# Performance work log

Hardware: AMD Instinct MI355X
Metric: run time of the kernel (lower is better)

The kernel has to match this reference:

```python
import jax, jax.numpy as jnp
import numpy as np

BS, C, H, W = 2, 128, 80, 160
P, G = 9, 8
GC = C // G
EPS = 1e-5


def _layernorm_c(x, g, b):
    # x: (bs, C, H, W); LayerNorm over channel dim (to_3d dim=2 -> norm over c)
    m = jnp.mean(x, axis=1, keepdims=True)
    v = jnp.mean((x - m) ** 2, axis=1, keepdims=True)
    return (x - m) / jnp.sqrt(v + EPS) * g[None, :, None, None] + b[None, :, None, None]


def _conv1x1(x, w, b):
    return jnp.einsum('bchw,oc->bohw', x, w) + b[None, :, None, None]


def _bilinear_sample(feat, pts):
    # feat (bs,C,H,W); pts (bs,N,2) normalized [0,1]; zero padding outside (DAF convention)
    bs, c, h, w = feat.shape
    x = pts[..., 0] * w - 0.5
    y = pts[..., 1] * h - 0.5
    x0 = jnp.floor(x)
    y0 = jnp.floor(y)
    dx = x - x0
    dy = y - y0
    x0i = x0.astype(jnp.int32)
    y0i = y0.astype(jnp.int32)

    def corner(xi, yi, wgt):
        valid = (xi >= 0) & (xi < w) & (yi >= 0) & (yi < h)
        xc = jnp.clip(xi, 0, w - 1)
        yc = jnp.clip(yi, 0, h - 1)
        g = jax.vmap(lambda f, yy, xx: f[:, yy, xx].T)(feat, yc, xc)  # (bs,N,C)
        return g * (wgt * valid)[..., None]

    return (corner(x0i, y0i, (1 - dx) * (1 - dy))
            + corner(x0i + 1, y0i, dx * (1 - dy))
            + corner(x0i, y0i + 1, (1 - dx) * dy)
            + corner(x0i + 1, y0i + 1, dx * dy))


def _branch(match_flat, anchor, feat_value, wmap, kp_w, kp_b):
    bs = feat_value.shape[0]
    hw = H * W
    # Sparse1DKeyPointsGenerator: learned 1D offsets along the disparity (x) direction
    off = match_flat @ kp_w.T + kp_b  # (bs, HW, P)
    anc = anchor.reshape(bs, hw, P, 2)
    kp = jnp.stack([anc[..., 0] + off, anc[..., 1]], axis=-1)  # (bs,HW,P,2)
    # group-softmax attention weights over num_pts
    wts = wmap.transpose(0, 2, 3, 1).reshape(bs, hw, P, G)  # channel c = p*G + g
    wts = jax.nn.softmax(wts, axis=2)
    # deformable aggregation: bilinear gather at key points + group-weighted sum over pts
    sampled = _bilinear_sample(feat_value, kp.reshape(bs, hw * P, 2))
    sampled = sampled.reshape(bs, hw, P, G, GC)
    out = jnp.einsum('bnpgc,bnpg->bngc', sampled, wts).reshape(bs, hw, C)
    out = out.reshape(bs, H, W, C).transpose(0, 3, 1, 2)
    return out, kp


def _forward(mask, match, context, geometric, context_anchor_points, geometric_anchor_points,
             ln_g, ln_b, lnc_g, lnc_b, lng_g, lng_b,
             wc_w, wc_b, wg_w, wg_b, vc_w, vc_b, vg_w, vg_b,
             out_w, out_b, kpc_w, kpc_b, kpg_w, kpg_b):
    bs = match.shape[0]
    hw = H * W
    match_n = _layernorm_c(match, ln_g, ln_b)
    context_n = _layernorm_c(context, lnc_g, lnc_b)
    geometric_n = _layernorm_c(geometric, lng_g, lng_b)
    ctx_val = _conv1x1(context_n, vc_w, vc_b)
    geo_val = _conv1x1(geometric_n, vg_w, vg_b)
    match_flat = match_n.reshape(bs, C, hw).transpose(0, 2, 1)  # (bs,HW,C)
    wc = _conv1x1(match_n, wc_w, wc_b)  # (bs,G*P,H,W)
    wg = _conv1x1(match_n, wg_w, wg_b)
    ctx_out, ctx_kp = _branch(match_flat, context_anchor_points, ctx_val, wc, kpc_w, kpc_b)
    geo_out, geo_kp = _branch(match_flat, geometric_anchor_points, geo_val, wg, kpg_w, kpg_b)
    out = jnp.concatenate([ctx_out * mask, geo_out], axis=1)
    out = _conv1x1(out, out_w, out_b)  # proj_drop is identity (p=0)
    return out, ctx_kp.reshape(bs, H, W, P, 2), geo_kp.reshape(bs, H, W, P, 2)


def setup_inputs() -> dict:
    key = jax.random.key(0)
    ks = jax.random.split(key, 20)

    def wn(k, shape):
        return jax.random.normal(k, shape, jnp.float32) * 0.02

    return {
        'mask': jax.random.uniform(ks[0], (BS, 1, H, W), jnp.float32),
        'match': jax.random.normal(ks[1], (BS, C, H, W), jnp.float32),
        'context': jax.random.normal(ks[2], (BS, C, H, W), jnp.float32),
        'geometric': jax.random.normal(ks[3], (BS, C, H, W), jnp.float32),
        'context_anchor_points': jax.random.uniform(ks[4], (BS, H, W, P, 2), jnp.float32),
        'geometric_anchor_points': jax.random.uniform(ks[5], (BS, H, W, P, 2), jnp.float32),
        'ln_g': jnp.ones((C,), jnp.float32), 'ln_b': jnp.zeros((C,), jnp.float32),
        'lnc_g': jnp.ones((C,), jnp.float32), 'lnc_b': jnp.zeros((C,), jnp.float32),
        'lng_g': jnp.ones((C,), jnp.float32), 'lng_b': jnp.zeros((C,), jnp.float32),
        'wc_w': wn(ks[6], (G * P, C)), 'wc_b': jnp.zeros((G * P,), jnp.float32),
        'wg_w': wn(ks[7], (G * P, C)), 'wg_b': jnp.zeros((G * P,), jnp.float32),
        'vc_w': wn(ks[8], (C, C)), 'vc_b': jnp.zeros((C,), jnp.float32),
        'vg_w': wn(ks[9], (C, C)), 'vg_b': jnp.zeros((C,), jnp.float32),
        'out_w': wn(ks[10], (C, 2 * C)), 'out_b': jnp.zeros((C,), jnp.float32),
        'kpc_w': wn(ks[11], (P, C)), 'kpc_b': jnp.zeros((P,), jnp.float32),
        'kpg_w': wn(ks[12], (P, C)), 'kpg_b': jnp.zeros((P,), jnp.float32),
    }


def reference(mask, match, context, geometric, context_anchor_points, geometric_anchor_points,
              ln_g, ln_b, lnc_g, lnc_b, lng_g, lng_b,
              wc_w, wc_b, wg_w, wg_b, vc_w, vc_b, vg_w, vg_b,
              out_w, out_b, kpc_w, kpc_b, kpg_w, kpg_b):
    return _forward(mask, match, context, geometric, context_anchor_points, geometric_anchor_points,
                    ln_g, ln_b, lnc_g, lnc_b, lng_g, lng_b,
                    wc_w, wc_b, wg_w, wg_b, vc_w, vc_b, vg_w, vg_b,
                    out_w, out_b, kpc_w, kpc_b, kpg_w, kpg_b)
```

## Files before the change

### kernel.cpp

```cpp
#include <hip/hip_runtime.h>
#include <hip/hip_bf16.h>

typedef __hip_bfloat16 bf16;
typedef __bf16 b16x8 __attribute__((ext_vector_type(8)));
typedef float f32x4 __attribute__((ext_vector_type(4)));

#define HWs   12800
#define NPIX  25600
#define IMG_H 80
#define IMG_W 160

static __device__ inline b16x8 load_w8(const float* p)
{
    const float4* q = (const float4*)p;
    float4 a = q[0], b = q[1];
    b16x8 r;
    r[0] = (__bf16)a.x; r[1] = (__bf16)a.y; r[2] = (__bf16)a.z; r[3] = (__bf16)a.w;
    r[4] = (__bf16)b.x; r[5] = (__bf16)b.y; r[6] = (__bf16)b.z; r[7] = (__bf16)b.w;
    return r;
}

__global__ __launch_bounds__(256) void k_stage1(
    const float* __restrict__ match, const float* __restrict__ context, const float* __restrict__ geometric,
    const float* __restrict__ ln_g, const float* __restrict__ ln_b,
    const float* __restrict__ lnc_g, const float* __restrict__ lnc_b,
    const float* __restrict__ lng_g, const float* __restrict__ lng_b,
    const float* __restrict__ vc_w, const float* __restrict__ vc_b,
    const float* __restrict__ vg_w, const float* __restrict__ vg_b,
    const float* __restrict__ wc_w, const float* __restrict__ wc_b,
    const float* __restrict__ wg_w, const float* __restrict__ wg_b,
    const float* __restrict__ kpc_w, const float* __restrict__ kpc_b,
    const float* __restrict__ kpg_w, const float* __restrict__ kpg_b,
    const float* __restrict__ anc_c, const float* __restrict__ anc_g,
    bf16* __restrict__ ctx_val, bf16* __restrict__ geo_val,
    bf16* __restrict__ wts_g, float* __restrict__ coords_g,
    float* __restrict__ kp_out)
{
    __shared__ __align__(16) bf16 tile_s[32 * 136];
    __shared__ bf16 logit_s[32 * 144];
    __shared__ float offs_s[32 * 18];
    __shared__ float red1[8][32];
    __shared__ float red2[8][32];

    int bx = blockIdx.x;
    int seg = bx / 800;
    int tile = bx - seg * 800;
    int t = threadIdx.x;
    int pixbase = tile * 32;

    const float* X  = (seg == 0) ? context : (seg == 1) ? geometric : match;
    const float* gg = (seg == 0) ? lnc_g   : (seg == 1) ? lng_g     : ln_g;
    const float* bb = (seg == 0) ? lnc_b   : (seg == 1) ? lng_b     : ln_b;

    {
        int p = t & 31;
        int cq = t >> 5;
        int b = pixbase >= HWs;
        int hw = pixbase - b * HWs;
        const float* base = X + ((size_t)b * 128) * HWs + hw + p;
        float xv[16];
        float s1 = 0.f, s2 = 0.f;
#pragma unroll
        for (int j = 0; j < 16; j++) {
            int c = cq * 16 + j;
            float v = base[(size_t)c * HWs];
            xv[j] = v; s1 += v; s2 += v * v;
        }
        red1[cq][p] = s1; red2[cq][p] = s2;
        __syncthreads();
        float S1 = 0.f, S2 = 0.f;
#pragma unroll
        for (int q = 0; q < 8; q++) { S1 += red1[q][p]; S2 += red2[q][p]; }
        float mean = S1 * (1.f / 128.f);
        float var  = fmaxf(S2 * (1.f / 128.f) - mean * mean, 0.f);
        float rstd = rsqrtf(var + 1e-5f);
#pragma unroll
        for (int j = 0; j < 16; j++) {
            int c = cq * 16 + j;
            float y = (xv[j] - mean) * rstd * gg[c] + bb[c];
            tile_s[p * 136 + c] = __float2bfloat16(y);
        }
        __syncthreads();
    }

    int wv = t >> 6;
    int lane = t & 63;
    int s = wv >> 1;
    int h = wv & 1;
    int lrow = lane & 15;
    int lq = lane >> 4;
    const b16x8* arow = (const b16x8*)(tile_s + (s * 16 + lrow) * 136);
    b16x8 af[4];
#pragma unroll
    for (int kk = 0; kk < 4; kk++) af[kk] = arow[kk * 4 + lq];

    if (seg < 2) {
        const float* Wv = (seg == 0) ? vc_w : vg_w;
        const float* Bv = (seg == 0) ? vc_b : vg_b;
        bf16* val = (seg == 0) ? ctx_val : geo_val;
#pragma unroll
        for (int i = 0; i < 4; i++) {
            int o = (h + 2 * i) * 16 + lrow;
            const float* wrow = Wv + (size_t)o * 128;
            f32x4 acc = {0.f, 0.f, 0.f, 0.f};
#pragma unroll
            for (int kk = 0; kk < 4; kk++)
                acc = __builtin_amdgcn_mfma_f32_16x16x32_bf16(af[kk], load_w8(wrow + (kk * 4 + lq) * 8), acc, 0, 0, 0);
            float bias = Bv[o];
#pragma unroll
            for (int r = 0; r < 4; r++) {
                int pix = pixbase + s * 16 + lq * 4 + r;
                val[(size_t)pix * 128 + o] = __float2bfloat16(acc[r] + bias);
            }
        }
        return;
    }

    for (int ot = h; ot < 11; ot += 2) {
        int o = ot * 16 + lrow;
        const float* wr; float bias;
        if (o < 72)       { wr = wc_w  + (size_t)o * 128;         bias = wc_b[o]; }
        else if (o < 144) { wr = wg_w  + (size_t)(o - 72) * 128;  bias = wg_b[o - 72]; }
        else if (o < 153) { wr = kpc_w + (size_t)(o - 144) * 128; bias = kpc_b[o - 144]; }
        else if (o < 162) { wr = kpg_w + (size_t)(o - 153) * 128; bias = kpg_b[o - 153]; }
        else              { wr = kpg_w + (size_t)8 * 128;         bias = 0.f; }
        f32x4 acc = {0.f, 0.f, 0.f, 0.f};
#pragma unroll
        for (int kk = 0; kk < 4; kk++)
            acc = __builtin_amdgcn_mfma_f32_16x16x32_bf16(af[kk], load_w8(wr + (kk * 4 + lq) * 8), acc, 0, 0, 0);
#pragma unroll
        for (int r = 0; r < 4; r++) {
            int row = s * 16 + lq * 4 + r;
            float v = acc[r] + bias;
            if (o < 144)       logit_s[row * 144 + o] = __float2bfloat16(v);
            else if (o < 162)  offs_s[row * 18 + (o - 144)] = v;
        }
    }
    __syncthreads();

#pragma unroll
    for (int i = 0; i < 2; i++) {
        int task = t + 256 * i;
        int lp = task >> 4;
        int sub = task & 15;
        int br = sub >> 3;
        int g = sub & 7;
        const bf16* base = logit_s + lp * 144 + br * 72 + g;
        float v[9];
        float m = -1e30f;
#pragma unroll
        for (int p = 0; p < 9; p++) { v[p] = __bfloat162float(base[p * 8]); m = fmaxf(m, v[p]); }
        float ssum = 0.f;
#pragma unroll
        for (int p = 0; p < 9; p++) { v[p] = __expf(v[p] - m); ssum += v[p]; }
        float inv = 1.f / ssum;
        int pix = pixbase + lp;
        bf16* wb = wts_g + ((size_t)pix * 2 + br) * 72 + g * 9;
#pragma unroll
        for (int p = 0; p < 9; p++) wb[p] = __float2bfloat16(v[p] * inv);
    }

    for (int i = 0; i < 3; i++) {
        int task = t + 256 * i;
        if (task < 576) {
            int lp = task / 18;
            int sub = task - lp * 18;
            int br = sub / 9;
            int p = sub - br * 9;
            int pix = pixbase + lp;
            float off = offs_s[lp * 18 + br * 9 + p];
            const float* anc = br ? anc_g : anc_c;
            float ax = anc[(size_t)pix * 18 + p * 2];
            float ay = anc[(size_t)pix * 18 + p * 2 + 1];
            float kx = ax + off;
            float* kpo = kp_out + (size_t)br * (NPIX * 18) + (size_t)pix * 18 + p * 2;
            kpo[0] = kx;
            kpo[1] = ay;
            float* cbp = coords_g + ((size_t)pix * 2 + br) * 18 + p * 2;
            cbp[0] = kx * 160.f - 0.5f;
            cbp[1] = ay * 80.f - 0.5f;
        }
    }
}

__global__ __launch_bounds__(256) void k_agg(
    const bf16* __restrict__ ctx_val, const bf16* __restrict__ geo_val,
    const bf16* __restrict__ wts_g, const float* __restrict__ coords_g,
    const float* __restrict__ mask,
    bf16* __restrict__ aggf)
{
    int t = threadIdx.x;
    int wv = t >> 6;
    int lane = t & 63;
    int q = lane >> 4;
    int sub = lane & 15;
    int c0 = sub * 8;
    int g = sub >> 1;

    int bx = blockIdx.x;
    int xcd = bx & 7;
    int br = xcd >> 2;
    int grp = (bx >> 3) * 4 + (xcd & 3);
    int pix = grp * 16 + wv * 4 + q;
    int tk = pix * 2 + br;
    int b = pix >= HWs;
    int rowbase = b * HWs;

    const bf16* val = br ? geo_val : ctx_val;
    const float* cb = coords_g + (size_t)tk * 18;
    const bf16* wb = wts_g + (size_t)tk * 72 + g * 9;

    float wtv[9];
#pragma unroll
    for (int p = 0; p < 9; p++) wtv[p] = __bfloat162float(wb[p]);

    float acc[8] = {0.f, 0.f, 0.f, 0.f, 0.f, 0.f, 0.f, 0.f};
    for (int p = 0; p < 9; p++) {
        float px = cb[p * 2];
        float py = cb[p * 2 + 1];
        float fx = floorf(px), fy = floorf(py);
        float dx = px - fx, dy = py - fy;
        int x0 = (int)fx, y0 = (int)fy;
        float wt = wtv[p];
#pragma unroll
        for (int c4 = 0; c4 < 4; c4++) {
            int xi = x0 + (c4 & 1);
            int yi = y0 + (c4 >> 1);
            bool ok = (xi >= 0) & (xi < IMG_W) & (yi >= 0) & (yi < IMG_H);
            int xc = min(max(xi, 0), IMG_W - 1);
            int yc = min(max(yi, 0), IMG_H - 1);
            float wx = (c4 & 1) ? dx : 1.f - dx;
            float wy = (c4 >> 1) ? dy : 1.f - dy;
            float wgt = ok ? wx * wy * wt : 0.f;
            b16x8 v = *(const b16x8*)(val + (size_t)(rowbase + yc * IMG_W + xc) * 128 + c0);
#pragma unroll
            for (int j = 0; j < 8; j++) acc[j] += wgt * (float)v[j];
        }
    }
    float mv = (br == 0) ? mask[pix] : 1.f;
    b16x8 pk;
#pragma unroll
    for (int j = 0; j < 8; j++) pk[j] = (__bf16)(acc[j] * mv);
    *(b16x8*)(aggf + (size_t)pix * 256 + br * 128 + c0) = pk;
}

__global__ __launch_bounds__(256) void k_gemm_out(
    const bf16* __restrict__ aggf,
    const float* __restrict__ out_w, const float* __restrict__ out_b,
    float* __restrict__ out)
{
    int t = threadIdx.x;
    int pixbase = blockIdx.x * 32;
    int wv = t >> 6;
    int lane = t & 63;
    int s = wv >> 1;
    int h = wv & 1;
    int lrow = lane & 15;
    int lq = lane >> 4;
    const b16x8* arow = (const b16x8*)(aggf + (size_t)(pixbase + s * 16 + lrow) * 256);
    b16x8 af[8];
#pragma unroll
    for (int kk = 0; kk < 8; kk++) af[kk] = arow[kk * 4 + lq];
    int b = pixbase >= HWs;
#pragma unroll
    for (int i = 0; i < 4; i++) {
        int o = (h + 2 * i) * 16 + lrow;
        const float* wrow = out_w + (size_t)o * 256;
        f32x4 acc = {0.f, 0.f, 0.f, 0.f};
#pragma unroll
        for (int kk = 0; kk < 8; kk++)
            acc = __builtin_amdgcn_mfma_f32_16x16x32_bf16(af[kk], load_w8(wrow + (kk * 4 + lq) * 8), acc, 0, 0, 0);
        float bias = out_b[o];
#pragma unroll
        for (int r = 0; r < 4; r++) {
            int pix = pixbase + s * 16 + lq * 4 + r;
            int hw = pix - b * HWs;
            out[(size_t)b * (128 * HWs) + (size_t)o * HWs + hw] = acc[r] + bias;
        }
    }
}

extern "C" void kernel_launch(void* const* d_in, const int* in_sizes, int n_in,
                              void* d_out, int out_size, void* d_ws, size_t ws_size,
                              hipStream_t stream)
{
    const float* mask      = (const float*)d_in[0];
    const float* match     = (const float*)d_in[1];
    const float* context   = (const float*)d_in[2];
    const float* geometric = (const float*)d_in[3];
    const float* anc_c     = (const float*)d_in[4];
    const float* anc_g     = (const float*)d_in[5];
    const float* ln_g  = (const float*)d_in[6];
    const float* ln_b  = (const float*)d_in[7];
    const float* lnc_g = (const float*)d_in[8];
    const float* lnc_b = (const float*)d_in[9];
    const float* lng_g = (const float*)d_in[10];
    const float* lng_b = (const float*)d_in[11];
    const float* wc_w  = (const float*)d_in[12];
    const float* wc_b  = (const float*)d_in[13];
    const float* wg_w  = (const float*)d_in[14];
    const float* wg_b  = (const float*)d_in[15];
    const float* vc_w  = (const float*)d_in[16];
    const float* vc_b  = (const float*)d_in[17];
    const float* vg_w  = (const float*)d_in[18];
    const float* vg_b  = (const float*)d_in[19];
    const float* out_w = (const float*)d_in[20];
    const float* out_b = (const float*)d_in[21];
    const float* kpc_w = (const float*)d_in[22];
    const float* kpc_b = (const float*)d_in[23];
    const float* kpg_w = (const float*)d_in[24];
    const float* kpg_b = (const float*)d_in[25];

    char* w = (char*)d_ws;
    bf16*  ctx_val  = (bf16*)(w);
    bf16*  geo_val  = (bf16*)(w + 6553600);
    bf16*  wts_g    = (bf16*)(w + 13107200);
    float* coords_g = (float*)(w + 20480000);
    bf16*  aggf     = (bf16*)(w + 24166400);

    float* outp = (float*)d_out;
    float* kp_out = outp + (size_t)2 * 128 * HWs;

    k_stage1<<<2400, 256, 0, stream>>>(match, context, geometric,
                                       ln_g, ln_b, lnc_g, lnc_b, lng_g, lng_b,
                                       vc_w, vc_b, vg_w, vg_b,
                                       wc_w, wc_b, wg_w, wg_b,
                                       kpc_w, kpc_b, kpg_w, kpg_b,
                                       anc_c, anc_g,
                                       ctx_val, geo_val, wts_g, coords_g, kp_out);
    k_agg<<<3200, 256, 0, stream>>>(ctx_val, geo_val, wts_g, coords_g, mask, aggf);
    k_gemm_out<<<800, 256, 0, stream>>>(aggf, out_w, out_b, outp);
}
```

Baseline: 238.6 us.

## Pre-convert weights to bf16, prefetch them early, fuse aggregation with output GEMM

Adds a prep kernel that converts all projection weights to bf16 and packs the matched-branch weights and biases into one contiguous buffer. Stage 1 now loads its weight fragments before the LayerNorm reduction so the loads overlap with the input loads. The aggregation and output GEMM are fused into one kernel that keeps the aggregated features in shared memory, so the aggf buffer no longer goes to and from global memory. The fused kernel runs 800 blocks with four sampling tasks per thread, down from 3200 blocks, which reduces parallelism for the latency-bound gather and drops the old XCD-aware block mapping.

```diff
diff --git a/kernel.cpp b/kernel.cpp
--- a/kernel.cpp
+++ b/kernel.cpp
@@ -10,14 +10,45 @@
 #define IMG_H 80
 #define IMG_W 160
 
-static __device__ inline b16x8 load_w8(const float* p)
+#define OFF_VCB  0
+#define OFF_VGB  16384
+#define OFF_MATB 32768
+#define OFF_OUTB 53504
+#define NW_BF16  86272
+
+__global__ __launch_bounds__(256) void k_prep(
+    const float* __restrict__ vc_w, const float* __restrict__ vg_w,
+    const float* __restrict__ wc_w, const float* __restrict__ wg_w,
+    const float* __restrict__ kpc_w, const float* __restrict__ kpg_w,
+    const float* __restrict__ out_w,
+    const float* __restrict__ wc_b, const float* __restrict__ wg_b,
+    const float* __restrict__ kpc_b, const float* __restrict__ kpg_b,
+    bf16* __restrict__ wbuf, float* __restrict__ bias176)
 {
-    const float4* q = (const float4*)p;
-    float4 a = q[0], b = q[1];
-    b16x8 r;
-    r[0] = (__bf16)a.x; r[1] = (__bf16)a.y; r[2] = (__bf16)a.z; r[3] = (__bf16)a.w;
-    r[4] = (__bf16)b.x; r[5] = (__bf16)b.y; r[6] = (__bf16)b.z; r[7] = (__bf16)b.w;
-    return r;
+    int i = blockIdx.x * 256 + threadIdx.x;
+    if (i < 16384) {
+        wbuf[i] = __float2bfloat16(vc_w[i]);
+    } else if (i < 32768) {
+        wbuf[i] = __float2bfloat16(vg_w[i - 16384]);
+    } else if (i < 53504) {
+        int j = i - 32768; int row = j >> 7; int c = j & 127;
+        float v;
+        if (row < 72)       v = wc_w[row * 128 + c];
+        else if (row < 144) v = wg_w[(row - 72) * 128 + c];
+        else if (row < 153) v = kpc_w[(row - 144) * 128 + c];
+        else                v = kpg_w[(row - 153) * 128 + c];
+        wbuf[i] = __float2bfloat16(v);
+    } else if (i < NW_BF16) {
+        wbuf[i] = __float2bfloat16(out_w[i - 53504]);
+    } else if (i < NW_BF16 + 176) {
+        int j = i - NW_BF16;
+        float v = 0.f;
+        if (j < 72)       v = wc_b[j];
+        else if (j < 144) v = wg_b[j - 72];
+        else if (j < 153) v = kpc_b[j - 144];
+        else if (j < 162) v = kpg_b[j - 153];
+        bias176[j] = v;
+    }
 }
 
 __global__ __launch_bounds__(256) void k_stage1(
@@ -25,12 +56,8 @@
     const float* __restrict__ ln_g, const float* __restrict__ ln_b,
     const float* __restrict__ lnc_g, const float* __restrict__ lnc_b,
     const float* __restrict__ lng_g, const float* __restrict__ lng_b,
-    const float* __restrict__ vc_w, const float* __restrict__ vc_b,
-    const float* __restrict__ vg_w, const float* __restrict__ vg_b,
-    const float* __restrict__ wc_w, const float* __restrict__ wc_b,
-    const float* __restrict__ wg_w, const float* __restrict__ wg_b,
-    const float* __restrict__ kpc_w, const float* __restrict__ kpc_b,
-    const float* __restrict__ kpg_w, const float* __restrict__ kpg_b,
+    const float* __restrict__ vc_b, const float* __restrict__ vg_b,
+    const bf16* __restrict__ wbuf, const float* __restrict__ bias176,
     const float* __restrict__ anc_c, const float* __restrict__ anc_g,
     bf16* __restrict__ ctx_val, bf16* __restrict__ geo_val,
     bf16* __restrict__ wts_g, float* __restrict__ coords_g,
@@ -52,36 +79,14 @@
     const float* gg = (seg == 0) ? lnc_g   : (seg == 1) ? lng_g     : ln_g;
     const float* bb = (seg == 0) ? lnc_b   : (seg == 1) ? lng_b     : ln_b;
 
-    {
-        int p = t & 31;
-        int cq = t >> 5;
-        int b = pixbase >= HWs;
-        int hw = pixbase - b * HWs;
-        const float* base = X + ((size_t)b * 128) * HWs + hw + p;
-        float xv[16];
-        float s1 = 0.f, s2 = 0.f;
-#pragma unroll
-        for (int j = 0; j < 16; j++) {
-            int c = cq * 16 + j;
-            float v = base[(size_t)c * HWs];
-            xv[j] = v; s1 += v; s2 += v * v;
-        }
-        red1[cq][p] = s1; red2[cq][p] = s2;
-        __syncthreads();
-        float S1 = 0.f, S2 = 0.f;
-#pragma unroll
-        for (int q = 0; q < 8; q++) { S1 += red1[q][p]; S2 += red2[q][p]; }
-        float mean = S1 * (1.f / 128.f);
-        float var  = fmaxf(S2 * (1.f / 128.f) - mean * mean, 0.f);
-        float rstd = rsqrtf(var + 1e-5f);
-#pragma unroll
-        for (int j = 0; j < 16; j++) {
-            int c = cq * 16 + j;
-            float y = (xv[j] - mean) * rstd * gg[c] + bb[c];
-            tile_s[p * 136 + c] = __float2bfloat16(y);
-        }
-        __syncthreads();
-    }
+    int p = t & 31;
+    int cq = t >> 5;
+    int b = pixbase >= HWs;
+    int hw = pixbase - b * HWs;
+    const float* base = X + ((size_t)b * 128) * HWs + hw + p;
+    float xv[16];
+#pragma unroll
+    for (int j = 0; j < 16; j++) xv[j] = base[(size_t)(cq * 16 + j) * HWs];
 
     int wv = t >> 6;
     int lane = t & 63;
@@ -89,45 +94,86 @@
     int h = wv & 1;
     int lrow = lane & 15;
     int lq = lane >> 4;
+    const bf16* Wb = (seg == 0) ? wbuf + OFF_VCB
+                   : (seg == 1) ? wbuf + OFF_VGB
+                                : wbuf + OFF_MATB;
+    b16x8 wf[4][4];
+    float bpre[4];
+#pragma unroll
+    for (int i = 0; i < 4; i++) {
+        int o = (h + 2 * i) * 16 + lrow;
+        const bf16* wr = Wb + (size_t)o * 128;
+#pragma unroll
+        for (int kk = 0; kk < 4; kk++)
+            wf[i][kk] = *(const b16x8*)(wr + (kk * 4 + lq) * 8);
+        bpre[i] = (seg == 0) ? vc_b[o] : (seg == 1) ? vg_b[o] : bias176[o];
+    }
+
+    {
+        float s1 = 0.f, s2 = 0.f;
+#pragma unroll
+        for (int j = 0; j < 16; j++) { s1 += xv[j]; s2 += xv[j] * xv[j]; }
+        red1[cq][p] = s1; red2[cq][p] = s2;
+        __syncthreads();
+        float S1 = 0.f, S2 = 0.f;
+#pragma unroll
+        for (int q = 0; q < 8; q++) { S1 += red1[q][p]; S2 += red2[q][p]; }
+        float mean = S1 * (1.f / 128.f);
+        float var  = fmaxf(S2 * (1.f / 128.f) - mean * mean, 0.f);
+        float rstd = rsqrtf(var + 1e-5f);
+#pragma unroll
+        for (int j = 0; j < 16; j++) {
+            int c = cq * 16 + j;
+            float y = (xv[j] - mean) * rstd * gg[c] + bb[c];
+            tile_s[p * 136 + c] = __float2bfloat16(y);
+        }
+        __syncthreads();
+    }
+
     const b16x8* arow = (const b16x8*)(tile_s + (s * 16 + lrow) * 136);
     b16x8 af[4];
 #pragma unroll
     for (int kk = 0; kk < 4; kk++) af[kk] = arow[kk * 4 + lq];
 
     if (seg < 2) {
-        const float* Wv = (seg == 0) ? vc_w : vg_w;
-        const float* Bv = (seg == 0) ? vc_b : vg_b;
         bf16* val = (seg == 0) ? ctx_val : geo_val;
 #pragma unroll
         for (int i = 0; i < 4; i++) {
             int o = (h + 2 * i) * 16 + lrow;
-            const float* wrow = Wv + (size_t)o * 128;
             f32x4 acc = {0.f, 0.f, 0.f, 0.f};
 #pragma unroll
             for (int kk = 0; kk < 4; kk++)
-                acc = __builtin_amdgcn_mfma_f32_16x16x32_bf16(af[kk], load_w8(wrow + (kk * 4 + lq) * 8), acc, 0, 0, 0);
-            float bias = Bv[o];
+                acc = __builtin_amdgcn_mfma_f32_16x16x32_bf16(af[kk], wf[i][kk], acc, 0, 0, 0);
 #pragma unroll
             for (int r = 0; r < 4; r++) {
                 int pix = pixbase + s * 16 + lq * 4 + r;
-                val[(size_t)pix * 128 + o] = __float2bfloat16(acc[r] + bias);
+                val[(size_t)pix * 128 + o] = __float2bfloat16(acc[r] + bpre[i]);
             }
         }
         return;
     }
 
-    for (int ot = h; ot < 11; ot += 2) {
+#pragma unroll
+    for (int i = 0; i < 4; i++) {
+        int o = (h + 2 * i) * 16 + lrow;
+        f32x4 acc = {0.f, 0.f, 0.f, 0.f};
+#pragma unroll
+        for (int kk = 0; kk < 4; kk++)
+            acc = __builtin_amdgcn_mfma_f32_16x16x32_bf16(af[kk], wf[i][kk], acc, 0, 0, 0);
+#pragma unroll
+        for (int r = 0; r < 4; r++) {
+            int row = s * 16 + lq * 4 + r;
+            logit_s[row * 144 + o] = __float2bfloat16(acc[r] + bpre[i]);
+        }
+    }
+    for (int ot = h + 8; ot < 11; ot += 2) {
         int o = ot * 16 + lrow;
-        const float* wr; float bias;
-        if (o < 72)       { wr = wc_w  + (size_t)o * 128;         bias = wc_b[o]; }
-        else if (o < 144) { wr = wg_w  + (size_t)(o - 72) * 128;  bias = wg_b[o - 72]; }
-        else if (o < 153) { wr = kpc_w + (size_t)(o - 144) * 128; bias = kpc_b[o - 144]; }
-        else if (o < 162) { wr = kpg_w + (size_t)(o - 153) * 128; bias = kpg_b[o - 153]; }
-        else              { wr = kpg_w + (size_t)8 * 128;         bias = 0.f; }
+        const bf16* wr = Wb + (size_t)o * 128;
         f32x4 acc = {0.f, 0.f, 0.f, 0.f};
 #pragma unroll
         for (int kk = 0; kk < 4; kk++)
-            acc = __builtin_amdgcn_mfma_f32_16x16x32_bf16(af[kk], load_w8(wr + (kk * 4 + lq) * 8), acc, 0, 0, 0);
+            acc = __builtin_amdgcn_mfma_f32_16x16x32_bf16(af[kk], *(const b16x8*)(wr + (kk * 4 + lq) * 8), acc, 0, 0, 0);
+        float bias = bias176[o];
 #pragma unroll
         for (int r = 0; r < 4; r++) {
             int row = s * 16 + lq * 4 + r;
@@ -145,19 +191,19 @@
         int sub = task & 15;
         int br = sub >> 3;
         int g = sub & 7;
-        const bf16* base = logit_s + lp * 144 + br * 72 + g;
+        const bf16* basel = logit_s + lp * 144 + br * 72 + g;
         float v[9];
         float m = -1e30f;
 #pragma unroll
-        for (int p = 0; p < 9; p++) { v[p] = __bfloat162float(base[p * 8]); m = fmaxf(m, v[p]); }
+        for (int pp = 0; pp < 9; pp++) { v[pp] = __bfloat162float(basel[pp * 8]); m = fmaxf(m, v[pp]); }
         float ssum = 0.f;
 #pragma unroll
-        for (int p = 0; p < 9; p++) { v[p] = __expf(v[p] - m); ssum += v[p]; }
+        for (int pp = 0; pp < 9; pp++) { v[pp] = __expf(v[pp] - m); ssum += v[pp]; }
         float inv = 1.f / ssum;
         int pix = pixbase + lp;
-        bf16* wb = wts_g + ((size_t)pix * 2 + br) * 72 + g * 9;
-#pragma unroll
-        for (int p = 0; p < 9; p++) wb[p] = __float2bfloat16(v[p] * inv);
+        bf16* wbp = wts_g + ((size_t)pix * 2 + br) * 72 + g * 9;
+#pragma unroll
+        for (int pp = 0; pp < 9; pp++) wbp[pp] = __float2bfloat16(v[pp] * inv);
     }
 
     for (int i = 0; i < 3; i++) {
@@ -166,29 +212,31 @@
             int lp = task / 18;
             int sub = task - lp * 18;
             int br = sub / 9;
-            int p = sub - br * 9;
+            int pp = sub - br * 9;
             int pix = pixbase + lp;
-            float off = offs_s[lp * 18 + br * 9 + p];
+            float off = offs_s[lp * 18 + br * 9 + pp];
             const float* anc = br ? anc_g : anc_c;
-            float ax = anc[(size_t)pix * 18 + p * 2];
-            float ay = anc[(size_t)pix * 18 + p * 2 + 1];
+            float ax = anc[(size_t)pix * 18 + pp * 2];
+            float ay = anc[(size_t)pix * 18 + pp * 2 + 1];
             float kx = ax + off;
-            float* kpo = kp_out + (size_t)br * (NPIX * 18) + (size_t)pix * 18 + p * 2;
+            float* kpo = kp_out + (size_t)br * (NPIX * 18) + (size_t)pix * 18 + pp * 2;
             kpo[0] = kx;
             kpo[1] = ay;
-            float* cbp = coords_g + ((size_t)pix * 2 + br) * 18 + p * 2;
+            float* cbp = coords_g + ((size_t)pix * 2 + br) * 18 + pp * 2;
             cbp[0] = kx * 160.f - 0.5f;
             cbp[1] = ay * 80.f - 0.5f;
         }
     }
 }
 
-__global__ __launch_bounds__(256) void k_agg(
+__global__ __launch_bounds__(256) void k_aggout(
     const bf16* __restrict__ ctx_val, const bf16* __restrict__ geo_val,
     const bf16* __restrict__ wts_g, const float* __restrict__ coords_g,
     const float* __restrict__ mask,
-    bf16* __restrict__ aggf)
+    const bf16* __restrict__ outb, const float* __restrict__ out_b,
+    float* __restrict__ out)
 {
+    __shared__ __align__(16) bf16 smem[32 * 264];
     int t = threadIdx.x;
     int wv = t >> 6;
     int lane = t & 63;
@@ -196,80 +244,70 @@
     int sub = lane & 15;
     int c0 = sub * 8;
     int g = sub >> 1;
-
-    int bx = blockIdx.x;
-    int xcd = bx & 7;
-    int br = xcd >> 2;
-    int grp = (bx >> 3) * 4 + (xcd & 3);
-    int pix = grp * 16 + wv * 4 + q;
-    int tk = pix * 2 + br;
-    int b = pix >= HWs;
+    int pixbase = blockIdx.x * 32;
+    int b = pixbase >= HWs;
     int rowbase = b * HWs;
-
-    const bf16* val = br ? geo_val : ctx_val;
-    const float* cb = coords_g + (size_t)tk * 18;
-    const bf16* wb = wts_g + (size_t)tk * 72 + g * 9;
-
-    float wtv[9];
-#pragma unroll
-    for (int p = 0; p < 9; p++) wtv[p] = __bfloat162float(wb[p]);
-
-    float acc[8] = {0.f, 0.f, 0.f, 0.f, 0.f, 0.f, 0.f, 0.f};
-    for (int p = 0; p < 9; p++) {
-        float px = cb[p * 2];
-        float py = cb[p * 2 + 1];
-        float fx = floorf(px), fy = floorf(py);
-        float dx = px - fx, dy = py - fy;
-        int x0 = (int)fx, y0 = (int)fy;
-        float wt = wtv[p];
-#pragma unroll
-        for (int c4 = 0; c4 < 4; c4++) {
-            int xi = x0 + (c4 & 1);
-            int yi = y0 + (c4 >> 1);
-            bool ok = (xi >= 0) & (xi < IMG_W) & (yi >= 0) & (yi < IMG_H);
-            int xc = min(max(xi, 0), IMG_W - 1);
-            int yc = min(max(yi, 0), IMG_H - 1);
-            float wx = (c4 & 1) ? dx : 1.f - dx;
-            float wy = (c4 >> 1) ? dy : 1.f - dy;
-            float wgt = ok ? wx * wy * wt : 0.f;
-            b16x8 v = *(const b16x8*)(val + (size_t)(rowbase + yc * IMG_W + xc) * 128 + c0);
-#pragma unroll
-            for (int j = 0; j < 8; j++) acc[j] += wgt * (float)v[j];
-        }
-    }
-    float mv = (br == 0) ? mask[pix] : 1.f;
-    b16x8 pk;
-#pragma unroll
-    for (int j = 0; j < 8; j++) pk[j] = (__bf16)(acc[j] * mv);
-    *(b16x8*)(aggf + (size_t)pix * 256 + br * 128 + c0) = pk;
-}
-
-__global__ __launch_bounds__(256) void k_gemm_out(
-    const bf16* __restrict__ aggf,
-    const float* __restrict__ out_w, const float* __restrict__ out_b,
-    float* __restrict__ out)
-{
-    int t = threadIdx.x;
-    int pixbase = blockIdx.x * 32;
-    int wv = t >> 6;
-    int lane = t & 63;
+    int qwid = wv * 4 + q;
+
+    for (int i = 0; i < 4; i++) {
+        int task = i * 16 + qwid;
+        int lp = task >> 1;
+        int br = task & 1;
+        int pix = pixbase + lp;
+        int tk = pix * 2 + br;
+        const bf16* val = br ? geo_val : ctx_val;
+        const float* cb = coords_g + (size_t)tk * 18;
+        const bf16* wb = wts_g + (size_t)tk * 72 + g * 9;
+        float wtv[9];
+#pragma unroll
+        for (int pp = 0; pp < 9; pp++) wtv[pp] = __bfloat162float(wb[pp]);
+        float acc[8] = {0.f, 0.f, 0.f, 0.f, 0.f, 0.f, 0.f, 0.f};
+        for (int pp = 0; pp < 9; pp++) {
+            float px = cb[pp * 2];
+            float py = cb[pp * 2 + 1];
+            float fx = floorf(px), fy = floorf(py);
+            float dx = px - fx, dy = py - fy;
+            int x0 = (int)fx, y0 = (int)fy;
+            float wt = wtv[pp];
+#pragma unroll
+            for (int c4 = 0; c4 < 4; c4++) {
+                int xi = x0 + (c4 & 1);
+                int yi = y0 + (c4 >> 1);
+                bool ok = (xi >= 0) & (xi < IMG_W) & (yi >= 0) & (yi < IMG_H);
+                int xc = min(max(xi, 0), IMG_W - 1);
+                int yc = min(max(yi, 0), IMG_H - 1);
+                float wx = (c4 & 1) ? dx : 1.f - dx;
+                float wy = (c4 >> 1) ? dy : 1.f - dy;
+                float wgt = ok ? wx * wy * wt : 0.f;
+                b16x8 v = *(const b16x8*)(val + (size_t)(rowbase + yc * IMG_W + xc) * 128 + c0);
+#pragma unroll
+                for (int j = 0; j < 8; j++) acc[j] += wgt * (float)v[j];
+            }
+        }
+        float mv = (br == 0) ? mask[pix] : 1.f;
+        b16x8 pk;
+#pragma unroll
+        for (int j = 0; j < 8; j++) pk[j] = (__bf16)(acc[j] * mv);
+        *(b16x8*)(smem + lp * 264 + br * 128 + c0) = pk;
+    }
+    __syncthreads();
+
     int s = wv >> 1;
     int h = wv & 1;
     int lrow = lane & 15;
     int lq = lane >> 4;
-    const b16x8* arow = (const b16x8*)(aggf + (size_t)(pixbase + s * 16 + lrow) * 256);
+    const b16x8* arow = (const b16x8*)(smem + (s * 16 + lrow) * 264);
     b16x8 af[8];
 #pragma unroll
     for (int kk = 0; kk < 8; kk++) af[kk] = arow[kk * 4 + lq];
-    int b = pixbase >= HWs;
 #pragma unroll
     for (int i = 0; i < 4; i++) {
         int o = (h + 2 * i) * 16 + lrow;
-        const float* wrow = out_w + (size_t)o * 256;
+        const bf16* wrow = outb + (size_t)o * 256;
         f32x4 acc = {0.f, 0.f, 0.f, 0.f};
 #pragma unroll
         for (int kk = 0; kk < 8; kk++)
-            acc = __builtin_amdgcn_mfma_f32_16x16x32_bf16(af[kk], load_w8(wrow + (kk * 4 + lq) * 8), acc, 0, 0, 0);
+            acc = __builtin_amdgcn_mfma_f32_16x16x32_bf16(af[kk], *(const b16x8*)(wrow + (kk * 4 + lq) * 8), acc, 0, 0, 0);
         float bias = out_b[o];
 #pragma unroll
         for (int r = 0; r < 4; r++) {
@@ -316,18 +354,20 @@
     bf16*  geo_val  = (bf16*)(w + 6553600);
     bf16*  wts_g    = (bf16*)(w + 13107200);
     float* coords_g = (float*)(w + 20480000);
-    bf16*  aggf     = (bf16*)(w + 24166400);
+    bf16*  wbuf     = (bf16*)(w + 24166400);
+    float* bias176  = (float*)(w + 24338944);
 
     float* outp = (float*)d_out;
     float* kp_out = outp + (size_t)2 * 128 * HWs;
 
+    k_prep<<<(NW_BF16 + 176 + 255) / 256, 256, 0, stream>>>(
+        vc_w, vg_w, wc_w, wg_w, kpc_w, kpg_w, out_w,
+        wc_b, wg_b, kpc_b, kpg_b, wbuf, bias176);
     k_stage1<<<2400, 256, 0, stream>>>(match, context, geometric,
                                        ln_g, ln_b, lnc_g, lnc_b, lng_g, lng_b,
-                                       vc_w, vc_b, vg_w, vg_b,
-                                       wc_w, wc_b, wg_w, wg_b,
-                                       kpc_w, kpc_b, kpg_w, kpg_b,
+                                       vc_b, vg_b, wbuf, bias176,
                                        anc_c, anc_g,
                                        ctx_val, geo_val, wts_g, coords_g, kp_out);
-    k_agg<<<3200, 256, 0, stream>>>(ctx_val, geo_val, wts_g, coords_g, mask, aggf);
-    k_gemm_out<<<800, 256, 0, stream>>>(aggf, out_w, out_b, outp);
+    k_aggout<<<800, 256, 0, stream>>>(ctx_val, geo_val, wts_g, coords_g, mask,
+                                      wbuf + OFF_OUTB, out_b, outp);
 }
```

Result: faster. 222.2 us (-6.9%).
